# Kernel tuning notes

Hardware: AMD Instinct MI355X
Metric: run time of the kernel (lower is better)

The kernel has to match this reference:

```python
import jax, jax.numpy as jnp
import numpy as np
from jax import lax

B, L, C_IN = 8, 4096, 9
D_MODEL, D_STATE, D_CONV, EXPAND, N_LAYERS = 128, 16, 4, 2, 2
D_INNER = EXPAND * D_MODEL
DT_RANK = (D_MODEL + 15) // 16  # 8, mamba default ceil(d_model/16)


def setup_inputs() -> dict:
    key = jax.random.key(0)
    ks = jax.random.split(key, 8)
    s = 0.02
    A_log = jnp.log(jnp.broadcast_to(
        jnp.arange(1, D_STATE + 1, dtype=jnp.float32), (N_LAYERS, D_INNER, D_STATE)))
    return {
        "t": jax.random.normal(ks[0], (B, L, C_IN), jnp.float32),
        "emb_w": jax.random.normal(ks[1], (D_MODEL, C_IN, 3), jnp.float32) * s,
        "in_proj_w": jax.random.normal(ks[2], (N_LAYERS, 2 * D_INNER, D_MODEL), jnp.float32) * s,
        "conv_w": jax.random.normal(ks[3], (N_LAYERS, D_INNER, D_CONV), jnp.float32) * s,
        "conv_b": jnp.zeros((N_LAYERS, D_INNER), jnp.float32),
        "x_proj_w": jax.random.normal(ks[4], (N_LAYERS, DT_RANK + 2 * D_STATE, D_INNER), jnp.float32) * s,
        "dt_proj_w": jax.random.normal(ks[5], (N_LAYERS, D_INNER, DT_RANK), jnp.float32) * (DT_RANK ** -0.5),
        "dt_proj_b": jnp.full((N_LAYERS, D_INNER), -4.6, jnp.float32),  # softplus^-1(~0.01)
        "A_log": A_log,
        "D": jnp.ones((N_LAYERS, D_INNER), jnp.float32),
        "out_proj_w": jax.random.normal(ks[6], (N_LAYERS, D_MODEL, D_INNER), jnp.float32) * s,
    }


def token_embed(t, w):
    # circular-padded Conv1d(c_in -> d_model, kernel=3, padding=1, bias=False)
    Lt = t.shape[1]
    xp = jnp.pad(t, ((0, 0), (1, 1), (0, 0)), mode="wrap")  # (B, L+2, c_in)
    out = jnp.zeros((t.shape[0], Lt, w.shape[0]), t.dtype)
    for k in range(3):
        out = out + jnp.einsum("blc,dc->bld", xp[:, k:k + Lt], w[:, :, k])
    return out


def selective_scan(u, dt, A, Bm, Cm, Dv):
    # u, dt: (B,L,d_in); Bm, Cm: (B,L,d_state); A: (d_in,d_state); Dv: (d_in,)
    h0 = jnp.zeros((u.shape[0], u.shape[2], A.shape[1]), u.dtype)

    def step(h, xs):
        dt_i, b_i, c_i, u_i = xs  # (B,d_in), (B,ds), (B,ds), (B,d_in)
        dA = jnp.exp(dt_i[..., None] * A)                      # (B,d_in,ds)
        h = dA * h + (dt_i * u_i)[..., None] * b_i[:, None, :]  # (B,d_in,ds)
        y = jnp.einsum("bds,bs->bd", h, c_i)
        return h, y

    _, ys = lax.scan(step, h0, (dt.swapaxes(0, 1), Bm.swapaxes(0, 1),
                                 Cm.swapaxes(0, 1), u.swapaxes(0, 1)))
    return ys.swapaxes(0, 1) + u * Dv  # (B,L,d_in)


def mamba_block(x, in_w, cw, cb, xp_w, dtw, dtb, A_log, Dv, ow):
    Lt = x.shape[1]
    xz = jnp.einsum("bld,ed->ble", x, in_w)            # (B,L,2*d_inner)
    xc, z = jnp.split(xz, 2, axis=-1)
    # causal depthwise conv1d (kernel d_conv) + bias + silu
    xpad = jnp.pad(xc, ((0, 0), (D_CONV - 1, 0), (0, 0)))
    conv = cb
    acc = jnp.zeros_like(xc)
    for k in range(D_CONV):
        acc = acc + xpad[:, k:k + Lt] * cw[:, k]
    xc = jax.nn.silu(acc + cb)
    # input-dependent dt, B, C
    dbl = jnp.einsum("bld,rd->blr", xc, xp_w)           # (B,L,dt_rank+2*ds)
    dt = dbl[..., :DT_RANK]
    Bm = dbl[..., DT_RANK:DT_RANK + D_STATE]
    Cm = dbl[..., DT_RANK + D_STATE:]
    dt = jax.nn.softplus(jnp.einsum("blr,dr->bld", dt, dtw) + dtb)
    A = -jnp.exp(A_log)
    y = selective_scan(xc, dt, A, Bm, Cm, Dv)
    y = y * jax.nn.silu(z)
    return jnp.einsum("bld,md->blm", y, ow)             # (B,L,d_model)


def reference(t, emb_w, in_proj_w, conv_w, conv_b, x_proj_w, dt_proj_w,
              dt_proj_b, A_log, D, out_proj_w):
    x = token_embed(t, emb_w)
    for i in range(N_LAYERS):
        x = mamba_block(x, in_proj_w[i], conv_w[i], conv_b[i], x_proj_w[i],
                        dt_proj_w[i], dt_proj_b[i], A_log[i], D[i], out_proj_w[i])
    pooled = x.mean(axis=1)  # AdaptiveAvgPool1d(1) over time + flatten -> (B, d_model)
    nrm = jnp.maximum(jnp.linalg.norm(pooled, axis=1, keepdims=True), 1e-12)
    return pooled / nrm
```

## Files before the change

### kernel.cpp

```cpp
#include <hip/hip_runtime.h>
#include <cmath>

#define LOG2E 1.4426950408889634f
#define LN2   0.6931471805599453f
#define C8    0.00390625f

constexpr int Bb = 8;
constexpr int Ll = 4096;
constexpr int Mrows = Bb * Ll;
constexpr int NC = 128;
constexpr int CL = Ll / NC;

typedef unsigned short u16;
typedef short s16x8 __attribute__((ext_vector_type(8)));
typedef float f32x4 __attribute__((ext_vector_type(4)));

__device__ __forceinline__ float hexp2(float x) { return __builtin_amdgcn_exp2f(x); }
__device__ __forceinline__ float hlog2(float x) { return __builtin_amdgcn_logf(x); }
__device__ __forceinline__ float hrcp(float x)  { return __builtin_amdgcn_rcpf(x); }

__device__ __forceinline__ float softplus_f(float x) {
  const float t = hexp2(-fabsf(x) * LOG2E);
  return fmaxf(x, 0.f) + LN2 * hlog2(1.f + t);
}
__device__ __forceinline__ float sigmoid_f(float x) {
  return hrcp(1.f + hexp2(-x * LOG2E));
}

__device__ __forceinline__ f32x4 mfma_bf(s16x8 a, s16x8 b, f32x4 c) {
  return __builtin_amdgcn_mfma_f32_16x16x32_bf16(a, b, c, 0, 0, 0);
}

__device__ __forceinline__ u16 bf16rne(float v) {
  unsigned u = __float_as_uint(v);
  u += 0x7FFFu + ((u >> 16) & 1u);
  return (u16)(u >> 16);
}
__device__ __forceinline__ float bf2f(u16 h) {
  return __uint_as_float(((unsigned)h) << 16);
}
__device__ __forceinline__ void split3(float v, u16& h, u16& m, u16& l) {
  h = bf16rne(v);
  const float r1 = (v - bf2f(h)) * 256.f;
  m = bf16rne(r1);
  const float r2 = (r1 - bf2f(m)) * 256.f;
  l = bf16rne(r2);
}

__global__ __launch_bounds__(256) void k_split3(const float* __restrict__ src,
                                                u16* __restrict__ h,
                                                u16* __restrict__ m,
                                                u16* __restrict__ l, int n) {
  const int i = blockIdx.x * 256 + threadIdx.x;
  if (i < n) {
    u16 a, b, c;
    split3(src[i], a, b, c);
    h[i] = a; m[i] = b; l[i] = c;
  }
}

__global__ __launch_bounds__(128) void k_embed(const float* __restrict__ t,
                                               const float* __restrict__ w,
                                               float* __restrict__ x) {
  __shared__ float ws[128 * 27];
  const int d = threadIdx.x;
  for (int i = d; i < 128 * 27; i += 128) ws[i] = w[i];
  __syncthreads();
  const int bpb = Ll / 32;
  const int b = blockIdx.x / bpb;
  const int l0 = (blockIdx.x % bpb) * 32;
  const float* wd = &ws[d * 27];
  for (int l = l0; l < l0 + 32; ++l) {
    float acc = 0.f;
#pragma unroll
    for (int k = 0; k < 3; ++k) {
      int li = l + k - 1;
      if (li < 0) li += Ll;
      if (li >= Ll) li -= Ll;
      const float* tr = t + ((size_t)b * Ll + li) * 9;
#pragma unroll
      for (int c = 0; c < 9; ++c) acc = fmaf(tr[c], wd[c * 3 + k], acc);
    }
    x[((size_t)b * Ll + l) * 128 + d] = acc;
  }
}

__global__ __launch_bounds__(512) void gemm3s(
    const float* __restrict__ A, int lda,
    const u16* __restrict__ Wh, const u16* __restrict__ Wm,
    const u16* __restrict__ Wl,
    float* __restrict__ C, int ldc, int N, int K) {
  __shared__ __align__(16) u16 Lh[128 * 40];
  __shared__ __align__(16) u16 Lm[128 * 40];
  __shared__ __align__(16) u16 Ll2[128 * 40];
  const int m0 = blockIdx.x * 128;
  const int n0 = blockIdx.y * 128;
  const int tid = threadIdx.x;
  const int lane = tid & 63;
  const int wid = tid >> 6;
  const int wm = wid & 1;
  const int wn = wid >> 1;
  const int lr = lane & 15;
  const int lq = lane >> 4;

  f32x4 a0[4][2], a1[4][2], a2[4][2];
  const f32x4 zz = {0.f, 0.f, 0.f, 0.f};
#pragma unroll
  for (int i = 0; i < 4; ++i)
#pragma unroll
    for (int j = 0; j < 2; ++j) { a0[i][j] = zz; a1[i][j] = zz; a2[i][j] = zz; }

  const int col0 = n0 + wn * 32 + lr;
  const int col1 = col0 + 16;
  const int c0 = col0 < N ? col0 : N - 1;
  const int c1 = col1 < N ? col1 : N - 1;
  const size_t bo0 = (size_t)c0 * K + lq * 8;
  const size_t bo1 = (size_t)c1 * K + lq * 8;

  const int srow = tid >> 2;
  const int sg = (tid & 3) * 8;
  const float* pa = A + (size_t)(m0 + srow) * lda + sg;
  const int sdst = srow * 40 + sg;

  for (int k0 = 0; k0 < K; k0 += 32) {
    const float4 va = *(const float4*)(pa + k0);
    const float4 vb = *(const float4*)(pa + k0 + 4);
    s16x8 h8, m8, l8;
    {
      u16 h, m, l;
      split3(va.x, h, m, l); h8[0] = (short)h; m8[0] = (short)m; l8[0] = (short)l;
      split3(va.y, h, m, l); h8[1] = (short)h; m8[1] = (short)m; l8[1] = (short)l;
      split3(va.z, h, m, l); h8[2] = (short)h; m8[2] = (short)m; l8[2] = (short)l;
      split3(va.w, h, m, l); h8[3] = (short)h; m8[3] = (short)m; l8[3] = (short)l;
      split3(vb.x, h, m, l); h8[4] = (short)h; m8[4] = (short)m; l8[4] = (short)l;
      split3(vb.y, h, m, l); h8[5] = (short)h; m8[5] = (short)m; l8[5] = (short)l;
      split3(vb.z, h, m, l); h8[6] = (short)h; m8[6] = (short)m; l8[6] = (short)l;
      split3(vb.w, h, m, l); h8[7] = (short)h; m8[7] = (short)m; l8[7] = (short)l;
    }
    *(s16x8*)&Lh[sdst] = h8;
    *(s16x8*)&Lm[sdst] = m8;
    *(s16x8*)&Ll2[sdst] = l8;
    __syncthreads();
    const s16x8 bh0 = *(const s16x8*)(Wh + bo0 + k0);
    const s16x8 bh1 = *(const s16x8*)(Wh + bo1 + k0);
    const s16x8 bm0 = *(const s16x8*)(Wm + bo0 + k0);
    const s16x8 bm1 = *(const s16x8*)(Wm + bo1 + k0);
    const s16x8 bl0 = *(const s16x8*)(Wl + bo0 + k0);
    const s16x8 bl1 = *(const s16x8*)(Wl + bo1 + k0);
#pragma unroll
    for (int mf = 0; mf < 4; ++mf) {
      const int ar = (wm * 64 + mf * 16 + lr) * 40 + lq * 8;
      const s16x8 ah = *(const s16x8*)&Lh[ar];
      const s16x8 am = *(const s16x8*)&Lm[ar];
      const s16x8 al = *(const s16x8*)&Ll2[ar];
      a0[mf][0] = mfma_bf(ah, bh0, a0[mf][0]);
      a1[mf][0] = mfma_bf(ah, bm0, a1[mf][0]);
      a1[mf][0] = mfma_bf(am, bh0, a1[mf][0]);
      a2[mf][0] = mfma_bf(ah, bl0, a2[mf][0]);
      a2[mf][0] = mfma_bf(al, bh0, a2[mf][0]);
      a2[mf][0] = mfma_bf(am, bm0, a2[mf][0]);
      a0[mf][1] = mfma_bf(ah, bh1, a0[mf][1]);
      a1[mf][1] = mfma_bf(ah, bm1, a1[mf][1]);
      a1[mf][1] = mfma_bf(am, bh1, a1[mf][1]);
      a2[mf][1] = mfma_bf(ah, bl1, a2[mf][1]);
      a2[mf][1] = mfma_bf(al, bh1, a2[mf][1]);
      a2[mf][1] = mfma_bf(am, bm1, a2[mf][1]);
    }
    __syncthreads();
  }
#pragma unroll
  for (int mf = 0; mf < 4; ++mf) {
#pragma unroll
    for (int nf = 0; nf < 2; ++nf) {
      const int col = n0 + wn * 32 + nf * 16 + lr;
      if (col < N) {
#pragma unroll
        for (int r = 0; r < 4; ++r) {
          const int row = m0 + wm * 64 + mf * 16 + lq * 4 + r;
          C[(size_t)row * ldc + col] =
              fmaf(C8, fmaf(C8, a2[mf][nf][r], a1[mf][nf][r]), a0[mf][nf][r]);
        }
      }
    }
  }
}

__global__ __launch_bounds__(256) void k_conv_silu(const float* __restrict__ xz,
                                                   const float* __restrict__ cw,
                                                   const float* __restrict__ cb,
                                                   float* __restrict__ u) {
  const int idx = blockIdx.x * 256 + threadIdx.x;
  const int d = idx & 255;
  const int bl = idx >> 8;
  const int l = bl & (Ll - 1);
  const float4 wv = *(const float4*)(cw + d * 4);
  float acc = 0.f;
  if (l >= 3) {
    acc = fmaf(xz[((size_t)(bl - 3)) * 512 + d], wv.x, acc);
    acc = fmaf(xz[((size_t)(bl - 2)) * 512 + d], wv.y, acc);
    acc = fmaf(xz[((size_t)(bl - 1)) * 512 + d], wv.z, acc);
    acc = fmaf(xz[((size_t)(bl - 0)) * 512 + d], wv.w, acc);
  } else {
    if (l >= 2) acc = fmaf(xz[((size_t)(bl - 2)) * 512 + d], wv.y, acc);
    if (l >= 1) acc = fmaf(xz[((size_t)(bl - 1)) * 512 + d], wv.z, acc);
    acc = fmaf(xz[((size_t)bl) * 512 + d], wv.w, acc);
  }
  acc += cb[d];
  u[idx] = acc * sigmoid_f(acc);
}

#define LOAD_A2(base)                                                        \
  float4 a2a = *(const float4*)((base));                                     \
  float4 a2b = *(const float4*)((base) + 4);                                 \
  float4 a2c = *(const float4*)((base) + 8);                                 \
  float4 a2d = *(const float4*)((base) + 12);                                \
  a2a.x = -expf(a2a.x) * LOG2E; a2a.y = -expf(a2a.y) * LOG2E;                \
  a2a.z = -expf(a2a.z) * LOG2E; a2a.w = -expf(a2a.w) * LOG2E;                \
  a2b.x = -expf(a2b.x) * LOG2E; a2b.y = -expf(a2b.y) * LOG2E;                \
  a2b.z = -expf(a2b.z) * LOG2E; a2b.w = -expf(a2b.w) * LOG2E;                \
  a2c.x = -expf(a2c.x) * LOG2E; a2c.y = -expf(a2c.y) * LOG2E;                \
  a2c.z = -expf(a2c.z) * LOG2E; a2c.w = -expf(a2c.w) * LOG2E;                \
  a2d.x = -expf(a2d.x) * LOG2E; a2d.y = -expf(a2d.y) * LOG2E;                \
  a2d.z = -expf(a2d.z) * LOG2E; a2d.w = -expf(a2d.w) * LOG2E;

#define DT_FROM_Q(q0, q1, w0, w1, dtbv)                                      \
  float dtr = (dtbv);                                                        \
  dtr = fmaf((q0).x, (w0).x, dtr); dtr = fmaf((q0).y, (w0).y, dtr);          \
  dtr = fmaf((q0).z, (w0).z, dtr); dtr = fmaf((q0).w, (w0).w, dtr);          \
  dtr = fmaf((q1).x, (w1).x, dtr); dtr = fmaf((q1).y, (w1).y, dtr);          \
  dtr = fmaf((q1).z, (w1).z, dtr); dtr = fmaf((q1).w, (w1).w, dtr);

#define UPD1(H, A, Bv)                                                       \
  (H).x = fmaf(hexp2(sp * (A).x), (H).x, dtu * (Bv).x);                      \
  (H).y = fmaf(hexp2(sp * (A).y), (H).y, dtu * (Bv).y);                      \
  (H).z = fmaf(hexp2(sp * (A).z), (H).z, dtu * (Bv).z);                      \
  (H).w = fmaf(hexp2(sp * (A).w), (H).w, dtu * (Bv).w);

#define UPD3(H, A, Bv, Cv)                                                   \
  (H).x = fmaf(hexp2(sp * (A).x), (H).x, dtu * (Bv).x);                      \
  y = fmaf((H).x, (Cv).x, y);                                                \
  (H).y = fmaf(hexp2(sp * (A).y), (H).y, dtu * (Bv).y);                      \
  y = fmaf((H).y, (Cv).y, y);                                                \
  (H).z = fmaf(hexp2(sp * (A).z), (H).z, dtu * (Bv).z);                      \
  y = fmaf((H).z, (Cv).z, y);                                                \
  (H).w = fmaf(hexp2(sp * (A).w), (H).w, dtu * (Bv).w);                      \
  y = fmaf((H).w, (Cv).w, y);

__global__ __launch_bounds__(256) void k_scan_ph1(
    const float* __restrict__ u, const float* __restrict__ dbl,
    const float* __restrict__ dtw, const float* __restrict__ dtb,
    const float* __restrict__ alog, float* __restrict__ hloc,
    float* __restrict__ sdtc) {
  const int b = blockIdx.x / NC;
  const int c = blockIdx.x % NC;
  const int d = threadIdx.x;
  LOAD_A2(alog + d * 16)
  const float4 w0 = *(const float4*)(dtw + d * 8);
  const float4 w1 = *(const float4*)(dtw + d * 8 + 4);
  const float dtbv = dtb[d];
  float4 ha = make_float4(0.f, 0.f, 0.f, 0.f);
  float4 hb = ha, hc = ha, hd = ha;
  float sdt = 0.f;
  const float* ub = u + (size_t)b * Ll * 256 + d;
  const float* db = dbl + (size_t)b * Ll * 40;
  const int l0 = c * CL;
  for (int l = l0; l < l0 + CL; ++l) {
    const float uv = ub[(size_t)l * 256];
    const float* dr = db + (size_t)l * 40;
    const float4 q0 = *(const float4*)(dr);
    const float4 q1 = *(const float4*)(dr + 4);
    const float4 bfa = *(const float4*)(dr + 8);
    const float4 bfb = *(const float4*)(dr + 12);
    const float4 bfc = *(const float4*)(dr + 16);
    const float4 bfd = *(const float4*)(dr + 20);
    DT_FROM_Q(q0, q1, w0, w1, dtbv)
    const float sp = softplus_f(dtr);
    sdt += sp;
    const float dtu = sp * uv;
    UPD1(ha, a2a, bfa)
    UPD1(hb, a2b, bfb)
    UPD1(hc, a2c, bfc)
    UPD1(hd, a2d, bfd)
  }
  const size_t o = (size_t)(b * NC + c) * 256 + d;
  *(float4*)(hloc + o * 16 + 0)  = ha;
  *(float4*)(hloc + o * 16 + 4)  = hb;
  *(float4*)(hloc + o * 16 + 8)  = hc;
  *(float4*)(hloc + o * 16 + 12) = hd;
  sdtc[o] = sdt;
}

__global__ __launch_bounds__(256) void k_scan_ph2(
    const float* __restrict__ alog, float* __restrict__ hloc,
    const float* __restrict__ sdtc) {
  const int b = blockIdx.x >> 4;
  const int dg = blockIdx.x & 15;
  const int d = dg * 16 + (threadIdx.x >> 4);
  const int s = threadIdx.x & 15;
  const float A2 = -expf(alog[d * 16 + s]) * LOG2E;
  float hs = 0.f;
  for (int c = 0; c < NC; ++c) {
    const size_t o = (size_t)(b * NC + c) * 256 + d;
    const float tmp = hloc[o * 16 + s];
    hloc[o * 16 + s] = hs;
    hs = fmaf(hexp2(A2 * sdtc[o]), hs, tmp);
  }
}

__global__ __launch_bounds__(256) void k_scan_ph3(
    const float* __restrict__ u, const float* __restrict__ dbl,
    const float* __restrict__ dtw, const float* __restrict__ dtb,
    const float* __restrict__ alog, const float* __restrict__ Dv,
    const float* __restrict__ hstart, float* __restrict__ xz) {
  const int b = blockIdx.x / NC;
  const int c = blockIdx.x % NC;
  const int d = threadIdx.x;
  LOAD_A2(alog + d * 16)
  const float4 w0 = *(const float4*)(dtw + d * 8);
  const float4 w1 = *(const float4*)(dtw + d * 8 + 4);
  const float dtbv = dtb[d];
  const float Dd = Dv[d];
  const size_t o = (size_t)(b * NC + c) * 256 + d;
  float4 ha = *(const float4*)(hstart + o * 16 + 0);
  float4 hb = *(const float4*)(hstart + o * 16 + 4);
  float4 hc = *(const float4*)(hstart + o * 16 + 8);
  float4 hd = *(const float4*)(hstart + o * 16 + 12);
  const float* ub = u + (size_t)b * Ll * 256 + d;
  const float* db = dbl + (size_t)b * Ll * 40;
  const int l0 = c * CL;
  for (int l = l0; l < l0 + CL; ++l) {
    const float uv = ub[(size_t)l * 256];
    const float* dr = db + (size_t)l * 40;
    const float4 q0 = *(const float4*)(dr);
    const float4 q1 = *(const float4*)(dr + 4);
    const float4 bfa = *(const float4*)(dr + 8);
    const float4 bfb = *(const float4*)(dr + 12);
    const float4 bfc = *(const float4*)(dr + 16);
    const float4 bfd = *(const float4*)(dr + 20);
    const float4 cfa = *(const float4*)(dr + 24);
    const float4 cfb = *(const float4*)(dr + 28);
    const float4 cfc = *(const float4*)(dr + 32);
    const float4 cfd = *(const float4*)(dr + 36);
    DT_FROM_Q(q0, q1, w0, w1, dtbv)
    const float sp = softplus_f(dtr);
    const float dtu = sp * uv;
    float y = 0.f;
    UPD3(ha, a2a, bfa, cfa)
    UPD3(hb, a2b, bfb, cfb)
    UPD3(hc, a2c, bfc, cfc)
    UPD3(hd, a2d, bfd, cfd)
    y = fmaf(uv, Dd, y);
    const size_t row = ((size_t)b * Ll + l) * 512;
    const float zv = xz[row + 256 + d];
    xz[row + d] = y * (zv * sigmoid_f(zv));
  }
}

__global__ __launch_bounds__(128) void k_pool_part(const float* __restrict__ x,
                                                   float* __restrict__ part) {
  const int b = blockIdx.x >> 5;
  const int c = blockIdx.x & 31;
  const int m = threadIdx.x;
  const float* xb = x + (size_t)b * Ll * 128 + (size_t)c * 128 * 128 + m;
  float s = 0.f;
#pragma unroll 4
  for (int l = 0; l < 128; ++l) s += xb[(size_t)l * 128];
  part[(size_t)blockIdx.x * 128 + m] = s;
}

__global__ __launch_bounds__(128) void k_pool_fin(const float* __restrict__ part,
                                                  float* __restrict__ out) {
  const int b = blockIdx.x, m = threadIdx.x;
  float p = 0.f;
#pragma unroll
  for (int c = 0; c < 32; ++c) p += part[((size_t)b * 32 + c) * 128 + m];
  p *= (1.f / Ll);
  __shared__ float pm[128];
  __shared__ float sq[128];
  pm[m] = p;
  sq[m] = p * p;
  __syncthreads();
  for (int wd = 64; wd >= 1; wd >>= 1) {
    if (m < wd) sq[m] += sq[m + wd];
    __syncthreads();
  }
  out[b * 128 + m] = pm[m] / fmaxf(sqrtf(sq[0]), 1e-12f);
}

extern "C" void kernel_launch(void* const* d_in, const int* in_sizes, int n_in,
                              void* d_out, int out_size, void* d_ws, size_t ws_size,
                              hipStream_t stream) {
  (void)in_sizes; (void)n_in; (void)out_size; (void)ws_size;
  const float* t    = (const float*)d_in[0];
  const float* embw = (const float*)d_in[1];
  const float* inw  = (const float*)d_in[2];
  const float* cw   = (const float*)d_in[3];
  const float* cb   = (const float*)d_in[4];
  const float* xpw  = (const float*)d_in[5];
  const float* dtw  = (const float*)d_in[6];
  const float* dtb  = (const float*)d_in[7];
  const float* alog = (const float*)d_in[8];
  const float* Dv   = (const float*)d_in[9];
  const float* ow   = (const float*)d_in[10];

  float* wsf  = (float*)d_ws;
  float* xz   = wsf;
  float* xb   = xz + 16777216;
  float* ubuf = xb + 4194304;
  float* dblb = ubuf + 8388608;
  float* hloc = dblb + 1310720;
  float* sdtc = hloc + 4194304;
  float* pool = sdtc + 262144;
  float* wtb  = pool + 32768;
  u16* wih = (u16*)(wtb);
  u16* wim = (u16*)(wtb + 65536);
  u16* wil = (u16*)(wtb + 131072);
  u16* wxh = (u16*)(wtb + 196608);
  u16* wxm = (u16*)(wtb + 206848);
  u16* wxl = (u16*)(wtb + 217088);
  u16* woh = (u16*)(wtb + 227328);
  u16* wom = (u16*)(wtb + 260096);
  u16* wol = (u16*)(wtb + 292864);
  float* outp = (float*)d_out;

  k_split3<<<dim3(512), 256, 0, stream>>>(inw, wih, wim, wil, 131072);
  k_split3<<<dim3(80),  256, 0, stream>>>(xpw, wxh, wxm, wxl, 20480);
  k_split3<<<dim3(256), 256, 0, stream>>>(ow,  woh, wom, wol, 65536);

  k_embed<<<dim3(Bb * (Ll / 32)), dim3(128), 0, stream>>>(t, embw, xb);

  for (int layer = 0; layer < 2; ++layer) {
    const u16* wih_l = wih + (size_t)layer * 512 * 128;
    const u16* wim_l = wim + (size_t)layer * 512 * 128;
    const u16* wil_l = wil + (size_t)layer * 512 * 128;
    const u16* wxh_l = wxh + (size_t)layer * 40 * 256;
    const u16* wxm_l = wxm + (size_t)layer * 40 * 256;
    const u16* wxl_l = wxl + (size_t)layer * 40 * 256;
    const u16* woh_l = woh + (size_t)layer * 128 * 256;
    const u16* wom_l = wom + (size_t)layer * 128 * 256;
    const u16* wol_l = wol + (size_t)layer * 128 * 256;
    const float* cw_l  = cw + layer * 256 * 4;
    const float* cb_l  = cb + layer * 256;
    const float* dtw_l = dtw + layer * 256 * 8;
    const float* dtb_l = dtb + layer * 256;
    const float* al_l  = alog + layer * 256 * 16;
    const float* D_l   = Dv + layer * 256;

    gemm3s<<<dim3(Mrows / 128, 4), 512, 0, stream>>>(
        xb, 128, wih_l, wim_l, wil_l, xz, 512, 512, 128);
    k_conv_silu<<<dim3(Mrows), 256, 0, stream>>>(xz, cw_l, cb_l, ubuf);
    gemm3s<<<dim3(Mrows / 128, 1), 512, 0, stream>>>(
        ubuf, 256, wxh_l, wxm_l, wxl_l, dblb, 40, 40, 256);
    k_scan_ph1<<<dim3(Bb * NC), 256, 0, stream>>>(ubuf, dblb, dtw_l, dtb_l,
                                                  al_l, hloc, sdtc);
    k_scan_ph2<<<dim3(Bb * 16), 256, 0, stream>>>(al_l, hloc, sdtc);
    k_scan_ph3<<<dim3(Bb * NC), 256, 0, stream>>>(ubuf, dblb, dtw_l, dtb_l,
                                                  al_l, D_l, hloc, xz);
    gemm3s<<<dim3(Mrows / 128, 1), 512, 0, stream>>>(
        xz, 512, woh_l, wom_l, wol_l, xb, 128, 128, 256);
  }

  k_pool_part<<<dim3(Bb * 32), 128, 0, stream>>>(xb, pool);
  k_pool_fin<<<dim3(Bb), 128, 0, stream>>>(pool, outp);
}
```

Before: 454.8 us.

## Fuse depthwise conv+SiLU into x_proj GEMM and scan kernels, shrink GEMM tiles

Removes the standalone conv+SiLU kernel and its u buffer. The conv is recomputed on the fly from xz inside the x_proj GEMM's A-tile load and inside both scan phases, using a rolling window of three previous inputs. The scan output now goes to a separate y buffer instead of being written back into xz. The GEMM tile also drops from 128 to 64 rows per block (256 threads), giving more blocks. The cost is redundant conv arithmetic and extra strided reads of xz in three kernels, traded against one fewer launch and less memory traffic.

```diff
diff --git a/kernel.cpp b/kernel.cpp
--- a/kernel.cpp
+++ b/kernel.cpp
@@ -25,6 +25,16 @@
 }
 __device__ __forceinline__ float sigmoid_f(float x) {
   return hrcp(1.f + hexp2(-x * LOG2E));
+}
+__device__ __forceinline__ float conv_u(float x3, float x2, float x1, float x0,
+                                        float4 w, float bias) {
+  float acc = 0.f;
+  acc = fmaf(x3, w.x, acc);
+  acc = fmaf(x2, w.y, acc);
+  acc = fmaf(x1, w.z, acc);
+  acc = fmaf(x0, w.w, acc);
+  acc += bias;
+  return acc * sigmoid_f(acc);
 }
 
 __device__ __forceinline__ f32x4 mfma_bf(s16x8 a, s16x8 b, f32x4 c) {
@@ -85,21 +95,21 @@
   }
 }
 
-__global__ __launch_bounds__(512) void gemm3s(
+template <bool FUSE>
+__global__ __launch_bounds__(256) void gemm3s(
     const float* __restrict__ A, int lda,
+    const float* __restrict__ cw, const float* __restrict__ cb,
     const u16* __restrict__ Wh, const u16* __restrict__ Wm,
     const u16* __restrict__ Wl,
     float* __restrict__ C, int ldc, int N, int K) {
-  __shared__ __align__(16) u16 Lh[128 * 40];
-  __shared__ __align__(16) u16 Lm[128 * 40];
-  __shared__ __align__(16) u16 Ll2[128 * 40];
-  const int m0 = blockIdx.x * 128;
+  __shared__ __align__(16) u16 Lh[64 * 40];
+  __shared__ __align__(16) u16 Lm[64 * 40];
+  __shared__ __align__(16) u16 Lo[64 * 40];
+  const int m0 = blockIdx.x * 64;
   const int n0 = blockIdx.y * 128;
   const int tid = threadIdx.x;
   const int lane = tid & 63;
-  const int wid = tid >> 6;
-  const int wm = wid & 1;
-  const int wn = wid >> 1;
+  const int wn = tid >> 6;
   const int lr = lane & 15;
   const int lq = lane >> 4;
 
@@ -119,27 +129,57 @@
 
   const int srow = tid >> 2;
   const int sg = (tid & 3) * 8;
-  const float* pa = A + (size_t)(m0 + srow) * lda + sg;
   const int sdst = srow * 40 + sg;
+  const int grow = m0 + srow;
 
   for (int k0 = 0; k0 < K; k0 += 32) {
-    const float4 va = *(const float4*)(pa + k0);
-    const float4 vb = *(const float4*)(pa + k0 + 4);
+    float v[8];
+    if constexpr (FUSE) {
+      const int l = grow & (Ll - 1);
+      const float* px = A + (size_t)grow * 512 + k0 + sg;
+      const float4 z4 = make_float4(0.f, 0.f, 0.f, 0.f);
+      float4 r0a = *(const float4*)px;
+      float4 r0b = *(const float4*)(px + 4);
+      float4 r1a = z4, r1b = z4, r2a = z4, r2b = z4, r3a = z4, r3b = z4;
+      if (l >= 1) { r1a = *(const float4*)(px - 512);  r1b = *(const float4*)(px - 508); }
+      if (l >= 2) { r2a = *(const float4*)(px - 1024); r2b = *(const float4*)(px - 1020); }
+      if (l >= 3) { r3a = *(const float4*)(px - 1536); r3b = *(const float4*)(px - 1532); }
+      const float* cwp = cw + (size_t)(k0 + sg) * 4;
+      const float4 w0 = *(const float4*)(cwp + 0);
+      const float4 w1 = *(const float4*)(cwp + 4);
+      const float4 w2 = *(const float4*)(cwp + 8);
+      const float4 w3 = *(const float4*)(cwp + 12);
+      const float4 w4 = *(const float4*)(cwp + 16);
+      const float4 w5 = *(const float4*)(cwp + 20);
+      const float4 w6 = *(const float4*)(cwp + 24);
+      const float4 w7 = *(const float4*)(cwp + 28);
+      const float4 cba = *(const float4*)(cb + k0 + sg);
+      const float4 cbb = *(const float4*)(cb + k0 + sg + 4);
+      v[0] = conv_u(r3a.x, r2a.x, r1a.x, r0a.x, w0, cba.x);
+      v[1] = conv_u(r3a.y, r2a.y, r1a.y, r0a.y, w1, cba.y);
+      v[2] = conv_u(r3a.z, r2a.z, r1a.z, r0a.z, w2, cba.z);
+      v[3] = conv_u(r3a.w, r2a.w, r1a.w, r0a.w, w3, cba.w);
+      v[4] = conv_u(r3b.x, r2b.x, r1b.x, r0b.x, w4, cbb.x);
+      v[5] = conv_u(r3b.y, r2b.y, r1b.y, r0b.y, w5, cbb.y);
+      v[6] = conv_u(r3b.z, r2b.z, r1b.z, r0b.z, w6, cbb.z);
+      v[7] = conv_u(r3b.w, r2b.w, r1b.w, r0b.w, w7, cbb.w);
+    } else {
+      const float* pa = A + (size_t)grow * lda + k0 + sg;
+      const float4 va = *(const float4*)pa;
+      const float4 vb = *(const float4*)(pa + 4);
+      v[0] = va.x; v[1] = va.y; v[2] = va.z; v[3] = va.w;
+      v[4] = vb.x; v[5] = vb.y; v[6] = vb.z; v[7] = vb.w;
+    }
     s16x8 h8, m8, l8;
-    {
+#pragma unroll
+    for (int j = 0; j < 8; ++j) {
       u16 h, m, l;
-      split3(va.x, h, m, l); h8[0] = (short)h; m8[0] = (short)m; l8[0] = (short)l;
-      split3(va.y, h, m, l); h8[1] = (short)h; m8[1] = (short)m; l8[1] = (short)l;
-      split3(va.z, h, m, l); h8[2] = (short)h; m8[2] = (short)m; l8[2] = (short)l;
-      split3(va.w, h, m, l); h8[3] = (short)h; m8[3] = (short)m; l8[3] = (short)l;
-      split3(vb.x, h, m, l); h8[4] = (short)h; m8[4] = (short)m; l8[4] = (short)l;
-      split3(vb.y, h, m, l); h8[5] = (short)h; m8[5] = (short)m; l8[5] = (short)l;
-      split3(vb.z, h, m, l); h8[6] = (short)h; m8[6] = (short)m; l8[6] = (short)l;
-      split3(vb.w, h, m, l); h8[7] = (short)h; m8[7] = (short)m; l8[7] = (short)l;
+      split3(v[j], h, m, l);
+      h8[j] = (short)h; m8[j] = (short)m; l8[j] = (short)l;
     }
     *(s16x8*)&Lh[sdst] = h8;
     *(s16x8*)&Lm[sdst] = m8;
-    *(s16x8*)&Ll2[sdst] = l8;
+    *(s16x8*)&Lo[sdst] = l8;
     __syncthreads();
     const s16x8 bh0 = *(const s16x8*)(Wh + bo0 + k0);
     const s16x8 bh1 = *(const s16x8*)(Wh + bo1 + k0);
@@ -149,10 +189,10 @@
     const s16x8 bl1 = *(const s16x8*)(Wl + bo1 + k0);
 #pragma unroll
     for (int mf = 0; mf < 4; ++mf) {
-      const int ar = (wm * 64 + mf * 16 + lr) * 40 + lq * 8;
+      const int ar = (mf * 16 + lr) * 40 + lq * 8;
       const s16x8 ah = *(const s16x8*)&Lh[ar];
       const s16x8 am = *(const s16x8*)&Lm[ar];
-      const s16x8 al = *(const s16x8*)&Ll2[ar];
+      const s16x8 al = *(const s16x8*)&Lo[ar];
       a0[mf][0] = mfma_bf(ah, bh0, a0[mf][0]);
       a1[mf][0] = mfma_bf(ah, bm0, a1[mf][0]);
       a1[mf][0] = mfma_bf(am, bh0, a1[mf][0]);
@@ -176,37 +216,13 @@
       if (col < N) {
 #pragma unroll
         for (int r = 0; r < 4; ++r) {
-          const int row = m0 + wm * 64 + mf * 16 + lq * 4 + r;
+          const int row = m0 + mf * 16 + lq * 4 + r;
           C[(size_t)row * ldc + col] =
               fmaf(C8, fmaf(C8, a2[mf][nf][r], a1[mf][nf][r]), a0[mf][nf][r]);
         }
       }
     }
   }
-}
-
-__global__ __launch_bounds__(256) void k_conv_silu(const float* __restrict__ xz,
-                                                   const float* __restrict__ cw,
-                                                   const float* __restrict__ cb,
-                                                   float* __restrict__ u) {
-  const int idx = blockIdx.x * 256 + threadIdx.x;
-  const int d = idx & 255;
-  const int bl = idx >> 8;
-  const int l = bl & (Ll - 1);
-  const float4 wv = *(const float4*)(cw + d * 4);
-  float acc = 0.f;
-  if (l >= 3) {
-    acc = fmaf(xz[((size_t)(bl - 3)) * 512 + d], wv.x, acc);
-    acc = fmaf(xz[((size_t)(bl - 2)) * 512 + d], wv.y, acc);
-    acc = fmaf(xz[((size_t)(bl - 1)) * 512 + d], wv.z, acc);
-    acc = fmaf(xz[((size_t)(bl - 0)) * 512 + d], wv.w, acc);
-  } else {
-    if (l >= 2) acc = fmaf(xz[((size_t)(bl - 2)) * 512 + d], wv.y, acc);
-    if (l >= 1) acc = fmaf(xz[((size_t)(bl - 1)) * 512 + d], wv.z, acc);
-    acc = fmaf(xz[((size_t)bl) * 512 + d], wv.w, acc);
-  }
-  acc += cb[d];
-  u[idx] = acc * sigmoid_f(acc);
 }
 
 #define LOAD_A2(base)                                                        \
@@ -247,7 +263,8 @@
   y = fmaf((H).w, (Cv).w, y);
 
 __global__ __launch_bounds__(256) void k_scan_ph1(
-    const float* __restrict__ u, const float* __restrict__ dbl,
+    const float* __restrict__ xz, const float* __restrict__ dbl,
+    const float* __restrict__ cw, const float* __restrict__ cb,
     const float* __restrict__ dtw, const float* __restrict__ dtb,
     const float* __restrict__ alog, float* __restrict__ hloc,
     float* __restrict__ sdtc) {
@@ -258,14 +275,21 @@
   const float4 w0 = *(const float4*)(dtw + d * 8);
   const float4 w1 = *(const float4*)(dtw + d * 8 + 4);
   const float dtbv = dtb[d];
+  const float4 cwd = *(const float4*)(cw + d * 4);
+  const float cbd = cb[d];
   float4 ha = make_float4(0.f, 0.f, 0.f, 0.f);
   float4 hb = ha, hc = ha, hd = ha;
   float sdt = 0.f;
-  const float* ub = u + (size_t)b * Ll * 256 + d;
+  const float* xb = xz + (size_t)b * Ll * 512 + d;
   const float* db = dbl + (size_t)b * Ll * 40;
   const int l0 = c * CL;
+  float x3 = l0 >= 3 ? xb[(size_t)(l0 - 3) * 512] : 0.f;
+  float x2 = l0 >= 2 ? xb[(size_t)(l0 - 2) * 512] : 0.f;
+  float x1 = l0 >= 1 ? xb[(size_t)(l0 - 1) * 512] : 0.f;
   for (int l = l0; l < l0 + CL; ++l) {
-    const float uv = ub[(size_t)l * 256];
+    const float x0 = xb[(size_t)l * 512];
+    const float uv = conv_u(x3, x2, x1, x0, cwd, cbd);
+    x3 = x2; x2 = x1; x1 = x0;
     const float* dr = db + (size_t)l * 40;
     const float4 q0 = *(const float4*)(dr);
     const float4 q1 = *(const float4*)(dr + 4);
@@ -308,10 +332,11 @@
 }
 
 __global__ __launch_bounds__(256) void k_scan_ph3(
-    const float* __restrict__ u, const float* __restrict__ dbl,
+    const float* __restrict__ xz, const float* __restrict__ dbl,
+    const float* __restrict__ cw, const float* __restrict__ cb,
     const float* __restrict__ dtw, const float* __restrict__ dtb,
     const float* __restrict__ alog, const float* __restrict__ Dv,
-    const float* __restrict__ hstart, float* __restrict__ xz) {
+    const float* __restrict__ hstart, float* __restrict__ ybuf) {
   const int b = blockIdx.x / NC;
   const int c = blockIdx.x % NC;
   const int d = threadIdx.x;
@@ -320,16 +345,24 @@
   const float4 w1 = *(const float4*)(dtw + d * 8 + 4);
   const float dtbv = dtb[d];
   const float Dd = Dv[d];
+  const float4 cwd = *(const float4*)(cw + d * 4);
+  const float cbd = cb[d];
   const size_t o = (size_t)(b * NC + c) * 256 + d;
   float4 ha = *(const float4*)(hstart + o * 16 + 0);
   float4 hb = *(const float4*)(hstart + o * 16 + 4);
   float4 hc = *(const float4*)(hstart + o * 16 + 8);
   float4 hd = *(const float4*)(hstart + o * 16 + 12);
-  const float* ub = u + (size_t)b * Ll * 256 + d;
+  const float* xb = xz + (size_t)b * Ll * 512 + d;
   const float* db = dbl + (size_t)b * Ll * 40;
+  float* yb = ybuf + (size_t)b * Ll * 256 + d;
   const int l0 = c * CL;
+  float x3 = l0 >= 3 ? xb[(size_t)(l0 - 3) * 512] : 0.f;
+  float x2 = l0 >= 2 ? xb[(size_t)(l0 - 2) * 512] : 0.f;
+  float x1 = l0 >= 1 ? xb[(size_t)(l0 - 1) * 512] : 0.f;
   for (int l = l0; l < l0 + CL; ++l) {
-    const float uv = ub[(size_t)l * 256];
+    const float x0 = xb[(size_t)l * 512];
+    const float uv = conv_u(x3, x2, x1, x0, cwd, cbd);
+    x3 = x2; x2 = x1; x1 = x0;
     const float* dr = db + (size_t)l * 40;
     const float4 q0 = *(const float4*)(dr);
     const float4 q1 = *(const float4*)(dr + 4);
@@ -350,9 +383,8 @@
     UPD3(hc, a2c, bfc, cfc)
     UPD3(hd, a2d, bfd, cfd)
     y = fmaf(uv, Dd, y);
-    const size_t row = ((size_t)b * Ll + l) * 512;
-    const float zv = xz[row + 256 + d];
-    xz[row + d] = y * (zv * sigmoid_f(zv));
+    const float zv = xb[(size_t)l * 512 + 256];
+    yb[(size_t)l * 256] = y * (zv * sigmoid_f(zv));
   }
 }
 
@@ -406,8 +438,8 @@
   float* wsf  = (float*)d_ws;
   float* xz   = wsf;
   float* xb   = xz + 16777216;
-  float* ubuf = xb + 4194304;
-  float* dblb = ubuf + 8388608;
+  float* ybuf = xb + 4194304;
+  float* dblb = ybuf + 8388608;
   float* hloc = dblb + 1310720;
   float* sdtc = hloc + 4194304;
   float* pool = sdtc + 262144;
@@ -446,18 +478,18 @@
     const float* al_l  = alog + layer * 256 * 16;
     const float* D_l   = Dv + layer * 256;
 
-    gemm3s<<<dim3(Mrows / 128, 4), 512, 0, stream>>>(
-        xb, 128, wih_l, wim_l, wil_l, xz, 512, 512, 128);
-    k_conv_silu<<<dim3(Mrows), 256, 0, stream>>>(xz, cw_l, cb_l, ubuf);
-    gemm3s<<<dim3(Mrows / 128, 1), 512, 0, stream>>>(
-        ubuf, 256, wxh_l, wxm_l, wxl_l, dblb, 40, 40, 256);
-    k_scan_ph1<<<dim3(Bb * NC), 256, 0, stream>>>(ubuf, dblb, dtw_l, dtb_l,
-                                                  al_l, hloc, sdtc);
+    gemm3s<false><<<dim3(Mrows / 64, 4), 256, 0, stream>>>(
+        xb, 128, nullptr, nullptr, wih_l, wim_l, wil_l, xz, 512, 512, 128);
+    gemm3s<true><<<dim3(Mrows / 64, 1), 256, 0, stream>>>(
+        xz, 512, cw_l, cb_l, wxh_l, wxm_l, wxl_l, dblb, 40, 40, 256);
+    k_scan_ph1<<<dim3(Bb * NC), 256, 0, stream>>>(xz, dblb, cw_l, cb_l,
+                                                  dtw_l, dtb_l, al_l, hloc, sdtc);
     k_scan_ph2<<<dim3(Bb * 16), 256, 0, stream>>>(al_l, hloc, sdtc);
-    k_scan_ph3<<<dim3(Bb * NC), 256, 0, stream>>>(ubuf, dblb, dtw_l, dtb_l,
-                                                  al_l, D_l, hloc, xz);
-    gemm3s<<<dim3(Mrows / 128, 1), 512, 0, stream>>>(
-        xz, 512, woh_l, wom_l, wol_l, xb, 128, 128, 256);
+    k_scan_ph3<<<dim3(Bb * NC), 256, 0, stream>>>(xz, dblb, cw_l, cb_l,
+                                                  dtw_l, dtb_l, al_l, D_l,
+                                                  hloc, ybuf);
+    gemm3s<false><<<dim3(Mrows / 64, 1), 256, 0, stream>>>(
+        ybuf, 256, nullptr, nullptr, woh_l, wom_l, wol_l, xb, 128, 128, 256);
   }
 
   k_pool_part<<<dim3(Bb * 32), 128, 0, stream>>>(xb, pool);
```

Result: faster. 416.3 us (-8.5%).
